# Optimization experiments

Hardware: AMD Instinct MI355X
Metric: run time of the kernel (lower is better)

The kernel has to match this reference:

```python
import jax, jax.numpy as jnp
import numpy as np
import math

N_HEAD = 16

def _rope(x):
    # x: [B, H, T, D], D even; interleaved-pair rotation as in the torch code
    B, H, T, D = x.shape
    theta = 10000.0 ** (-2.0 * jnp.arange(D // 2, dtype=x.dtype) / D)  # [D/2]
    pos = jnp.arange(T, dtype=x.dtype)[:, None]                        # [T,1]
    ang = pos * theta[None, :]                                          # [T, D/2]
    sin, cos = jnp.sin(ang), jnp.cos(ang)
    x1, x2 = x[..., ::2], x[..., 1::2]
    x1r = x1 * cos - x2 * sin
    x2r = x1 * sin + x2 * cos
    # re-interleave
    out = jnp.stack([x1r, x2r], axis=-1).reshape(B, H, T, D)
    return out

def setup_inputs() -> dict:
    key = jax.random.key(0)
    ks = jax.random.split(key, 3)
    B, T, C = 4, 2048, 1024
    x = jax.random.normal(ks[0], (B, T, C), dtype=jnp.float32)
    W_qkv = jax.random.normal(ks[1], (C, 3 * C), dtype=jnp.float32) * (1.0 / math.sqrt(C))
    b_qkv = jnp.zeros((3 * C,), dtype=jnp.float32)
    W_proj = jax.random.normal(ks[2], (C, C), dtype=jnp.float32) * (1.0 / math.sqrt(C))
    b_proj = jnp.zeros((C,), dtype=jnp.float32)
    return {"x": x, "W_qkv": W_qkv, "b_qkv": b_qkv, "W_proj": W_proj, "b_proj": b_proj}

def reference(x, W_qkv, b_qkv, W_proj, b_proj):
    B, T, C = x.shape
    H = N_HEAD
    D = C // H
    qkv = x @ W_qkv + b_qkv                      # [B,T,3C]
    q, k, v = jnp.split(qkv, 3, axis=-1)
    def to_heads(t):
        return t.reshape(B, T, H, D).transpose(0, 2, 1, 3)  # [B,H,T,D]
    q, k, v = to_heads(q), to_heads(k), to_heads(v)
    q = _rope(q)
    k = _rope(k)
    att = jnp.einsum('bhqd,bhkd->bhqk', q, k) * (1.0 / math.sqrt(D))
    mask = jnp.tril(jnp.ones((T, T), dtype=bool))
    att = jnp.where(mask[None, None, :, :], att, -jnp.inf)
    att = jax.nn.softmax(att, axis=-1)
    y = jnp.einsum('bhqk,bhkd->bhqd', att, v)    # [B,H,T,D]
    y = y.transpose(0, 2, 1, 3).reshape(B, T, C)
    return y @ W_proj + b_proj
```

## Files before the change

kernel.cpp:

```cpp
#include <hip/hip_runtime.h>
#include <cstddef>

#define B_DIM 4
#define T_DIM 2048
#define C_DIM 1024
#define H_DIM 16
#define D_DIM 64
#define C3_DIM 3072

typedef __attribute__((ext_vector_type(8))) _Float16 f16x8;
typedef __attribute__((ext_vector_type(4))) _Float16 f16x4;
typedef __attribute__((ext_vector_type(4))) float f32x4;

typedef const __attribute__((address_space(1))) unsigned int* gptr_t;
typedef __attribute__((address_space(3))) unsigned int* lptr_t;

#define QSCALE 0.180336850073f
#define NTHETA 0.41524101186f

__global__ __launch_bounds__(256) void prep(
    const float* __restrict__ x, _Float16* __restrict__ xh,
    const float* __restrict__ Wq, _Float16* __restrict__ Wqt,
    const float* __restrict__ Wp, _Float16* __restrict__ Wpt)
{
    __shared__ float tile[64][65];
    const int z = blockIdx.x, tid = threadIdx.x;

    if (z < 8192) {
        size_t i = (size_t)z * 1024 + tid * 4;
        float4 v = *(const float4*)&x[i];
        f16x4 o = { (_Float16)v.x, (_Float16)v.y, (_Float16)v.z, (_Float16)v.w };
        *(f16x4*)&xh[i] = o;
        return;
    }

    const float* W;
    _Float16* Wt;
    int N, idx;
    if (z < 8960) { W = Wq; Wt = Wqt; N = C3_DIM; idx = z - 8192; }
    else          { W = Wp; Wt = Wpt; N = C_DIM;  idx = z - 8960; }
    const int K = C_DIM;
    const int nblk = N / 64;
    const int n0 = (idx % nblk) * 64, k0 = (idx / nblk) * 64;

    const int tx = tid & 15, ty = tid >> 4;
#pragma unroll
    for (int it = 0; it < 4; ++it) {
        int r = it * 16 + ty;
        *(float4*)&tile[r][tx * 4] =
            *(const float4*)&W[(size_t)(k0 + r) * N + n0 + tx * 4];
    }
    __syncthreads();
    int c = tid >> 2, t0 = (tid & 3) * 16;
    __align__(16) _Float16 tmp[16];
#pragma unroll
    for (int j = 0; j < 16; ++j) tmp[j] = (_Float16)tile[t0 + j][c];
    _Float16* o = Wt + (size_t)(n0 + c) * K + k0 + t0;
    *(f16x8*)o = *(f16x8*)&tmp[0];
    *(f16x8*)(o + 8) = *(f16x8*)&tmp[8];
}

#define STAGE8(BUF, KK)                                                       \
    do {                                                                      \
        __builtin_amdgcn_global_load_lds((gptr_t)(const void*)(ag + (KK)),    \
            (lptr_t)(void*)&Af[BUF][0][w * 2 + 0][0][0], 16, 0, 0);           \
        __builtin_amdgcn_global_load_lds((gptr_t)(const void*)(ag + (KK) + 16 * K), \
            (lptr_t)(void*)&Af[BUF][0][w * 2 + 1][0][0], 16, 0, 0);           \
        __builtin_amdgcn_global_load_lds((gptr_t)(const void*)(ag + (KK) + 32), \
            (lptr_t)(void*)&Af[BUF][1][w * 2 + 0][0][0], 16, 0, 0);           \
        __builtin_amdgcn_global_load_lds((gptr_t)(const void*)(ag + (KK) + 32 + 16 * K), \
            (lptr_t)(void*)&Af[BUF][1][w * 2 + 1][0][0], 16, 0, 0);           \
        __builtin_amdgcn_global_load_lds((gptr_t)(const void*)(bg + (KK)),    \
            (lptr_t)(void*)&Bf[BUF][0][w * 2 + 0][0][0], 16, 0, 0);           \
        __builtin_amdgcn_global_load_lds((gptr_t)(const void*)(bg + (KK) + 16 * K), \
            (lptr_t)(void*)&Bf[BUF][0][w * 2 + 1][0][0], 16, 0, 0);           \
        __builtin_amdgcn_global_load_lds((gptr_t)(const void*)(bg + (KK) + 32), \
            (lptr_t)(void*)&Bf[BUF][1][w * 2 + 0][0][0], 16, 0, 0);           \
        __builtin_amdgcn_global_load_lds((gptr_t)(const void*)(bg + (KK) + 32 + 16 * K), \
            (lptr_t)(void*)&Bf[BUF][1][w * 2 + 1][0][0], 16, 0, 0);           \
    } while (0)

#define COMPUTE64(CUR, SWAPPED)                                               \
    do {                                                                      \
        _Pragma("unroll")                                                     \
        for (int s = 0; s < 2; ++s) {                                         \
            f16x8 av[4], bv[4];                                               \
            _Pragma("unroll")                                                 \
            for (int i = 0; i < 4; ++i) {                                     \
                av[i] = *(const f16x8*)&Af[CUR][s][wm * 4 + i][lane][0];      \
                bv[i] = *(const f16x8*)&Bf[CUR][s][wn * 4 + i][lane][0];      \
            }                                                                 \
            _Pragma("unroll")                                                 \
            for (int i = 0; i < 4; ++i)                                       \
                _Pragma("unroll")                                             \
                for (int j = 0; j < 4; ++j)                                   \
                    acc[i][j] = (SWAPPED)                                     \
                        ? __builtin_amdgcn_mfma_f32_16x16x32_f16(             \
                              bv[j], av[i], acc[i][j], 0, 0, 0)               \
                        : __builtin_amdgcn_mfma_f32_16x16x32_f16(             \
                              av[i], bv[j], acc[i][j], 0, 0, 0);              \
        }                                                                     \
    } while (0)

__global__ __launch_bounds__(256) void gemm_qkv(
    const _Float16* __restrict__ A, const _Float16* __restrict__ Bt,
    const float* __restrict__ bias,
    _Float16* __restrict__ Qb, _Float16* __restrict__ Kb, _Float16* __restrict__ Vt)
{
    __shared__ __align__(16) _Float16 Af[2][2][8][64][8];
    __shared__ __align__(16) _Float16 Bf[2][2][8][64][8];
    const int tid = threadIdx.x;
    const int lane = tid & 63, w = tid >> 6;
    const int lm = lane & 15, lq = lane >> 4;
    const int wm = w >> 1, wn = w & 1;
    const int m0 = blockIdx.y * 128, n0 = blockIdx.x * 128;
    const int K = C_DIM;

    const _Float16* ag = A + (size_t)(m0 + w * 32 + lm) * K + lq * 8;
    const _Float16* bg = Bt + (size_t)(n0 + w * 32 + lm) * K + lq * 8;

    f32x4 acc[4][4];
#pragma unroll
    for (int i = 0; i < 4; ++i)
#pragma unroll
        for (int j = 0; j < 4; ++j) acc[i][j] = (f32x4){0.f, 0.f, 0.f, 0.f};

    const bool is_v = (n0 >= 2 * C_DIM);

    if (!is_v) {
        STAGE8(0, 0);
        __syncthreads();
        int cur = 0;
        for (int kt = 0; kt < K / 64 - 1; ++kt) {
            STAGE8(cur ^ 1, (kt + 1) * 64);
            COMPUTE64(cur, true);
            __syncthreads();
            cur ^= 1;
        }
        COMPUTE64(cur, true);

        const bool is_q = (n0 < C_DIM);
        const float scale = is_q ? QSCALE : 1.0f;
        _Float16* dstbase = is_q ? Qb : Kb;
#pragma unroll
        for (int j = 0; j < 4; ++j) {
            int col = n0 + wn * 64 + j * 16 + lq * 4;
            int d0 = col & 63;
            int h = (col & (C_DIM - 1)) >> 6;
            float4 b4 = *(const float4*)&bias[col];
            float th0 = exp2f(-NTHETA * (float)(d0 >> 1));
            float th1 = exp2f(-NTHETA * (float)((d0 >> 1) + 1));
#pragma unroll
            for (int i = 0; i < 4; ++i) {
                int tg = m0 + wm * 64 + i * 16 + lm;
                int bb = tg >> 11, tl = tg & (T_DIM - 1);
                float v0 = acc[i][j][0] + b4.x;
                float v1 = acc[i][j][1] + b4.y;
                float v2 = acc[i][j][2] + b4.z;
                float v3 = acc[i][j][3] + b4.w;
                float s0, c0, s1, c1;
                __sincosf((float)tl * th0, &s0, &c0);
                __sincosf((float)tl * th1, &s1, &c1);
                f16x4 o = { (_Float16)((v0 * c0 - v1 * s0) * scale),
                            (_Float16)((v0 * s0 + v1 * c0) * scale),
                            (_Float16)((v2 * c1 - v3 * s1) * scale),
                            (_Float16)((v2 * s1 + v3 * c1) * scale) };
                *(f16x4*)&dstbase[((size_t)(bb * 16 + h) * T_DIM + tl) * 64 + d0] = o;
            }
        }
    } else {
        STAGE8(0, 0);
        __syncthreads();
        int cur = 0;
        for (int kt = 0; kt < K / 64 - 1; ++kt) {
            STAGE8(cur ^ 1, (kt + 1) * 64);
            COMPUTE64(cur, false);
            __syncthreads();
            cur ^= 1;
        }
        COMPUTE64(cur, false);

#pragma unroll
        for (int i = 0; i < 4; ++i) {
            int t4 = m0 + wm * 64 + i * 16 + lq * 4;
            int bb = t4 >> 11, tl = t4 & (T_DIM - 1);
#pragma unroll
            for (int j = 0; j < 4; ++j) {
                int col = n0 + wn * 64 + j * 16 + lm;
                int dfull = col - 2 * C_DIM;
                int h = dfull >> 6, d = dfull & 63;
                float bc = bias[col];
                f16x4 o = { (_Float16)(acc[i][j][0] + bc),
                            (_Float16)(acc[i][j][1] + bc),
                            (_Float16)(acc[i][j][2] + bc),
                            (_Float16)(acc[i][j][3] + bc) };
                *(f16x4*)&Vt[((size_t)(bb * 16 + h) * 64 + d) * T_DIM + tl] = o;
            }
        }
    }
}

template <bool OUT_HALF>
__global__ __launch_bounds__(256) void gemm_bt(
    const _Float16* __restrict__ A, const _Float16* __restrict__ Bt,
    const float* __restrict__ bias, void* __restrict__ Cout,
    int M, int N, int K)
{
    __shared__ __align__(16) _Float16 Af[2][2][8][64][8];
    __shared__ __align__(16) _Float16 Bf[2][2][8][64][8];
    const int tid = threadIdx.x;
    const int lane = tid & 63, w = tid >> 6;
    const int lm = lane & 15, lq = lane >> 4;
    const int wm = w >> 1, wn = w & 1;
    const int m0 = blockIdx.y * 128, n0 = blockIdx.x * 128;

    const _Float16* ag = A + (size_t)(m0 + w * 32 + lm) * K + lq * 8;
    const _Float16* bg = Bt + (size_t)(n0 + w * 32 + lm) * K + lq * 8;

    f32x4 acc[4][4];
#pragma unroll
    for (int i = 0; i < 4; ++i)
#pragma unroll
        for (int j = 0; j < 4; ++j) acc[i][j] = (f32x4){0.f, 0.f, 0.f, 0.f};

    STAGE8(0, 0);
    __syncthreads();
    int cur = 0;
    for (int kt = 0; kt < K / 64 - 1; ++kt) {
        STAGE8(cur ^ 1, (kt + 1) * 64);
        COMPUTE64(cur, true);
        __syncthreads();
        cur ^= 1;
    }
    COMPUTE64(cur, true);

#pragma unroll
    for (int i = 0; i < 4; ++i) {
        size_t row = (size_t)(m0 + wm * 64 + i * 16 + lm);
#pragma unroll
        for (int j = 0; j < 4; ++j) {
            int col = n0 + wn * 64 + j * 16 + lq * 4;
            float4 b4 = *(const float4*)&bias[col];
            float v0 = acc[i][j][0] + b4.x;
            float v1 = acc[i][j][1] + b4.y;
            float v2 = acc[i][j][2] + b4.z;
            float v3 = acc[i][j][3] + b4.w;
            if (OUT_HALF) {
                f16x4 o = { (_Float16)v0, (_Float16)v1, (_Float16)v2, (_Float16)v3 };
                *(f16x4*)&((_Float16*)Cout)[row * N + col] = o;
            } else {
                float4 o = make_float4(v0, v1, v2, v3);
                *(float4*)&((float*)Cout)[row * N + col] = o;
            }
        }
    }
}

__global__ __launch_bounds__(256) void attn_mfma(
    const _Float16* __restrict__ Qb, const _Float16* __restrict__ Kb,
    const _Float16* __restrict__ Vt, _Float16* __restrict__ yb)
{
    __shared__ __align__(16) _Float16 Kf[8][64][8];
    __shared__ __align__(16) _Float16 Vf[8][64][8];
    __shared__ __align__(16) _Float16 Pb[4][16][72];

    const int tid = threadIdx.x;
    const int bh = blockIdx.x;
    const int qt = 31 - blockIdx.y;
    const int b = bh >> 4, h = bh & 15;
    const int lane = tid & 63, w = tid >> 6;
    const int m = lane & 15, qq = lane >> 4;

    const _Float16* qrow = Qb +
        ((size_t)bh * T_DIM + qt * 64 + w * 16 + m) * D_DIM + qq * 8;
    f16x8 qreg[2];
    qreg[0] = *(const f16x8*)qrow;
    qreg[1] = *(const f16x8*)(qrow + 32);

    float m_i = -1e30f, l_i = 0.f;
    f32x4 acc[4];
#pragma unroll
    for (int db = 0; db < 4; ++db) acc[db] = (f32x4){0.f, 0.f, 0.f, 0.f};

    const _Float16* kg0 = Kb + (size_t)bh * T_DIM * D_DIM +
                          (size_t)(w * 16 + m) * D_DIM + qq * 8;
    const _Float16* vg0 = Vt + (size_t)bh * D_DIM * T_DIM +
                          (size_t)(w * 16 + m) * T_DIM + qq * 8;

    f16x8 kr0 = *(const f16x8*)(kg0);
    f16x8 kr1 = *(const f16x8*)(kg0 + 32);
    f16x8 vr0 = *(const f16x8*)(vg0);
    f16x8 vr1 = *(const f16x8*)(vg0 + 32);

    for (int kt = 0; kt <= qt; ++kt) {
        __syncthreads();
        *(f16x8*)&Kf[w * 2 + 0][lane][0] = kr0;
        *(f16x8*)&Kf[w * 2 + 1][lane][0] = kr1;
        *(f16x8*)&Vf[w * 2 + 0][lane][0] = vr0;
        *(f16x8*)&Vf[w * 2 + 1][lane][0] = vr1;
        __syncthreads();

        int ktn = (kt < qt) ? kt + 1 : kt;
        kr0 = *(const f16x8*)(kg0 + (size_t)ktn * 64 * D_DIM);
        kr1 = *(const f16x8*)(kg0 + (size_t)ktn * 64 * D_DIM + 32);
        vr0 = *(const f16x8*)(vg0 + ktn * 64);
        vr1 = *(const f16x8*)(vg0 + ktn * 64 + 32);

        f32x4 sv[4];
#pragma unroll
        for (int nb = 0; nb < 4; ++nb) {
            f32x4 s = (f32x4){0.f, 0.f, 0.f, 0.f};
            s = __builtin_amdgcn_mfma_f32_16x16x32_f16(
                *(const f16x8*)&Kf[nb * 2 + 0][lane][0], qreg[0], s, 0, 0, 0);
            s = __builtin_amdgcn_mfma_f32_16x16x32_f16(
                *(const f16x8*)&Kf[nb * 2 + 1][lane][0], qreg[1], s, 0, 0, 0);
            sv[nb] = s;
        }

        if (kt == qt) {
            int qlocal = w * 16 + m;
#pragma unroll
            for (int nb = 0; nb < 4; ++nb) {
                int tb = nb * 16 + qq * 4;
#pragma unroll
                for (int r = 0; r < 4; ++r)
                    if (tb + r > qlocal) sv[nb][r] = -1e30f;
            }
        }

        float mt0 = fmaxf(fmaxf(sv[0][0], sv[0][1]), fmaxf(sv[0][2], sv[0][3]));
        float mt1 = fmaxf(fmaxf(sv[1][0], sv[1][1]), fmaxf(sv[1][2], sv[1][3]));
        float mt2 = fmaxf(fmaxf(sv[2][0], sv[2][1]), fmaxf(sv[2][2], sv[2][3]));
        float mt3 = fmaxf(fmaxf(sv[3][0], sv[3][1]), fmaxf(sv[3][2], sv[3][3]));
        float mt = fmaxf(fmaxf(mt0, mt1), fmaxf(mt2, mt3));
        mt = fmaxf(mt, __shfl_xor(mt, 16));
        mt = fmaxf(mt, __shfl_xor(mt, 32));
        float mnew = fmaxf(m_i, mt);
        float alpha = exp2f(m_i - mnew);
        float ll = 0.f;
#pragma unroll
        for (int nb = 0; nb < 4; ++nb) {
            float p0 = exp2f(sv[nb][0] - mnew);
            float p1 = exp2f(sv[nb][1] - mnew);
            float p2 = exp2f(sv[nb][2] - mnew);
            float p3 = exp2f(sv[nb][3] - mnew);
            sv[nb][0] = p0; sv[nb][1] = p1; sv[nb][2] = p2; sv[nb][3] = p3;
            ll += (p0 + p1) + (p2 + p3);
        }
        ll += __shfl_xor(ll, 16);
        ll += __shfl_xor(ll, 32);
        l_i = l_i * alpha + ll;
        m_i = mnew;
#pragma unroll
        for (int db = 0; db < 4; ++db) {
            acc[db][0] *= alpha; acc[db][1] *= alpha;
            acc[db][2] *= alpha; acc[db][3] *= alpha;
        }

#pragma unroll
        for (int nb = 0; nb < 4; ++nb) {
            f16x4 pv = { (_Float16)sv[nb][0], (_Float16)sv[nb][1],
                         (_Float16)sv[nb][2], (_Float16)sv[nb][3] };
            *(f16x4*)&Pb[w][m][nb * 16 + qq * 4] = pv;
        }

        f16x8 pf0 = *(const f16x8*)&Pb[w][m][0 * 32 + qq * 8];
        f16x8 pf1 = *(const f16x8*)&Pb[w][m][1 * 32 + qq * 8];

#pragma unroll
        for (int db = 0; db < 4; ++db) {
            acc[db] = __builtin_amdgcn_mfma_f32_16x16x32_f16(
                *(const f16x8*)&Vf[db * 2 + 0][lane][0], pf0, acc[db], 0, 0, 0);
            acc[db] = __builtin_amdgcn_mfma_f32_16x16x32_f16(
                *(const f16x8*)&Vf[db * 2 + 1][lane][0], pf1, acc[db], 0, 0, 0);
        }
    }

    float inv = 1.0f / l_i;
    _Float16* yrow = yb + (size_t)(b * T_DIM + qt * 64 + w * 16 + m) * C_DIM +
                     h * D_DIM + qq * 4;
#pragma unroll
    for (int db = 0; db < 4; ++db) {
        f16x4 o = { (_Float16)(acc[db][0] * inv), (_Float16)(acc[db][1] * inv),
                    (_Float16)(acc[db][2] * inv), (_Float16)(acc[db][3] * inv) };
        *(f16x4*)(yrow + db * 16) = o;
    }
}

extern "C" void kernel_launch(void* const* d_in, const int* in_sizes, int n_in,
                              void* d_out, int out_size, void* d_ws, size_t ws_size,
                              hipStream_t stream)
{
    const float* x     = (const float*)d_in[0];
    const float* Wqkv  = (const float*)d_in[1];
    const float* bqkv  = (const float*)d_in[2];
    const float* Wproj = (const float*)d_in[3];
    const float* bproj = (const float*)d_in[4];
    float* out = (float*)d_out;

    char* ws = (char*)d_ws;
    _Float16* xh  = (_Float16*)(ws);
    _Float16* yh  = (_Float16*)(ws + 16777216ull);
    _Float16* Qb  = (_Float16*)(ws + 33554432ull);
    _Float16* Kb  = (_Float16*)(ws + 50331648ull);
    _Float16* Vt  = (_Float16*)(ws + 67108864ull);
    _Float16* Wqt = (_Float16*)(ws + 83886080ull);
    _Float16* Wpt = (_Float16*)(ws + 90177536ull);

    dim3 blk(256);

    prep<<<dim3(9216), blk, 0, stream>>>(x, xh, Wqkv, Wqt, Wproj, Wpt);

    gemm_qkv<<<dim3(C3_DIM / 128, (B_DIM * T_DIM) / 128), blk, 0, stream>>>(
        xh, Wqt, bqkv, Qb, Kb, Vt);

    attn_mfma<<<dim3(B_DIM * H_DIM, T_DIM / 64), blk, 0, stream>>>(
        Qb, Kb, Vt, yh);

    gemm_bt<false><<<dim3(C_DIM / 128, (B_DIM * T_DIM) / 128), blk, 0, stream>>>(
        yh, Wpt, bproj, out, B_DIM * T_DIM, C_DIM, C_DIM);
}
```

Measured before the change: 334.7 us.

## Halve GEMM k-tile to 32 and use partial vmcnt waits with raw barriers

Shrinks the per-stage K tile from 64 to 32, halving LDS usage per block, and rewrites the double-buffered main loop. It now issues the next stage's async global-to-LDS loads, waits only for the previous stage with a partial vmcnt, and syncs with raw s_barrier instead of __syncthreads. The aim is better overlap of loads with MFMA and possibly higher occupancy, at the cost of twice as many loop iterations and barriers per GEMM.

```diff
diff --git a/kernel.cpp b/kernel.cpp
--- a/kernel.cpp
+++ b/kernel.cpp
@@ -60,46 +60,54 @@
     *(f16x8*)(o + 8) = *(f16x8*)&tmp[8];
 }
 
-#define STAGE8(BUF, KK)                                                       \
+#define STAGE4(BUF, KK)                                                       \
     do {                                                                      \
         __builtin_amdgcn_global_load_lds((gptr_t)(const void*)(ag + (KK)),    \
-            (lptr_t)(void*)&Af[BUF][0][w * 2 + 0][0][0], 16, 0, 0);           \
-        __builtin_amdgcn_global_load_lds((gptr_t)(const void*)(ag + (KK) + 16 * K), \
-            (lptr_t)(void*)&Af[BUF][0][w * 2 + 1][0][0], 16, 0, 0);           \
-        __builtin_amdgcn_global_load_lds((gptr_t)(const void*)(ag + (KK) + 32), \
-            (lptr_t)(void*)&Af[BUF][1][w * 2 + 0][0][0], 16, 0, 0);           \
-        __builtin_amdgcn_global_load_lds((gptr_t)(const void*)(ag + (KK) + 32 + 16 * K), \
-            (lptr_t)(void*)&Af[BUF][1][w * 2 + 1][0][0], 16, 0, 0);           \
+            (lptr_t)(void*)&Af[BUF][w * 2 + 0][0][0], 16, 0, 0);              \
+        __builtin_amdgcn_global_load_lds(                                     \
+            (gptr_t)(const void*)(ag + (KK) + 16 * K),                        \
+            (lptr_t)(void*)&Af[BUF][w * 2 + 1][0][0], 16, 0, 0);              \
         __builtin_amdgcn_global_load_lds((gptr_t)(const void*)(bg + (KK)),    \
-            (lptr_t)(void*)&Bf[BUF][0][w * 2 + 0][0][0], 16, 0, 0);           \
-        __builtin_amdgcn_global_load_lds((gptr_t)(const void*)(bg + (KK) + 16 * K), \
-            (lptr_t)(void*)&Bf[BUF][0][w * 2 + 1][0][0], 16, 0, 0);           \
-        __builtin_amdgcn_global_load_lds((gptr_t)(const void*)(bg + (KK) + 32), \
-            (lptr_t)(void*)&Bf[BUF][1][w * 2 + 0][0][0], 16, 0, 0);           \
-        __builtin_amdgcn_global_load_lds((gptr_t)(const void*)(bg + (KK) + 32 + 16 * K), \
-            (lptr_t)(void*)&Bf[BUF][1][w * 2 + 1][0][0], 16, 0, 0);           \
+            (lptr_t)(void*)&Bf[BUF][w * 2 + 0][0][0], 16, 0, 0);              \
+        __builtin_amdgcn_global_load_lds(                                     \
+            (gptr_t)(const void*)(bg + (KK) + 16 * K),                        \
+            (lptr_t)(void*)&Bf[BUF][w * 2 + 1][0][0], 16, 0, 0);              \
     } while (0)
 
-#define COMPUTE64(CUR, SWAPPED)                                               \
+#define COMPUTE32(CUR, SWAPPED)                                               \
     do {                                                                      \
+        f16x8 av[4], bv[4];                                                   \
         _Pragma("unroll")                                                     \
-        for (int s = 0; s < 2; ++s) {                                         \
-            f16x8 av[4], bv[4];                                               \
+        for (int i = 0; i < 4; ++i) {                                         \
+            av[i] = *(const f16x8*)&Af[CUR][wm * 4 + i][lane][0];             \
+            bv[i] = *(const f16x8*)&Bf[CUR][wn * 4 + i][lane][0];             \
+        }                                                                     \
+        _Pragma("unroll")                                                     \
+        for (int i = 0; i < 4; ++i)                                           \
             _Pragma("unroll")                                                 \
-            for (int i = 0; i < 4; ++i) {                                     \
-                av[i] = *(const f16x8*)&Af[CUR][s][wm * 4 + i][lane][0];      \
-                bv[i] = *(const f16x8*)&Bf[CUR][s][wn * 4 + i][lane][0];      \
-            }                                                                 \
-            _Pragma("unroll")                                                 \
-            for (int i = 0; i < 4; ++i)                                       \
-                _Pragma("unroll")                                             \
-                for (int j = 0; j < 4; ++j)                                   \
-                    acc[i][j] = (SWAPPED)                                     \
-                        ? __builtin_amdgcn_mfma_f32_16x16x32_f16(             \
-                              bv[j], av[i], acc[i][j], 0, 0, 0)               \
-                        : __builtin_amdgcn_mfma_f32_16x16x32_f16(             \
-                              av[i], bv[j], acc[i][j], 0, 0, 0);              \
+            for (int j = 0; j < 4; ++j)                                       \
+                acc[i][j] = (SWAPPED)                                         \
+                    ? __builtin_amdgcn_mfma_f32_16x16x32_f16(                 \
+                          bv[j], av[i], acc[i][j], 0, 0, 0)                   \
+                    : __builtin_amdgcn_mfma_f32_16x16x32_f16(                 \
+                          av[i], bv[j], acc[i][j], 0, 0, 0);                  \
+    } while (0)
+
+#define KLOOP(SWAPPED)                                                        \
+    do {                                                                      \
+        STAGE4(0, 0);                                                         \
+        int cur = 0;                                                          \
+        for (int kt = 0; kt < K / 32 - 1; ++kt) {                             \
+            STAGE4(cur ^ 1, (kt + 1) * 32);                                   \
+            asm volatile("s_waitcnt vmcnt(4)" ::: "memory");                  \
+            __builtin_amdgcn_s_barrier();                                     \
+            COMPUTE32(cur, SWAPPED);                                          \
+            __builtin_amdgcn_s_barrier();                                     \
+            cur ^= 1;                                                         \
         }                                                                     \
+        asm volatile("s_waitcnt vmcnt(0)" ::: "memory");                      \
+        __builtin_amdgcn_s_barrier();                                         \
+        COMPUTE32(cur, SWAPPED);                                              \
     } while (0)
 
 __global__ __launch_bounds__(256) void gemm_qkv(
@@ -107,8 +115,8 @@
     const float* __restrict__ bias,
     _Float16* __restrict__ Qb, _Float16* __restrict__ Kb, _Float16* __restrict__ Vt)
 {
-    __shared__ __align__(16) _Float16 Af[2][2][8][64][8];
-    __shared__ __align__(16) _Float16 Bf[2][2][8][64][8];
+    __shared__ __align__(16) _Float16 Af[2][8][64][8];
+    __shared__ __align__(16) _Float16 Bf[2][8][64][8];
     const int tid = threadIdx.x;
     const int lane = tid & 63, w = tid >> 6;
     const int lm = lane & 15, lq = lane >> 4;
@@ -128,16 +136,7 @@
     const bool is_v = (n0 >= 2 * C_DIM);
 
     if (!is_v) {
-        STAGE8(0, 0);
-        __syncthreads();
-        int cur = 0;
-        for (int kt = 0; kt < K / 64 - 1; ++kt) {
-            STAGE8(cur ^ 1, (kt + 1) * 64);
-            COMPUTE64(cur, true);
-            __syncthreads();
-            cur ^= 1;
-        }
-        COMPUTE64(cur, true);
+        KLOOP(true);
 
         const bool is_q = (n0 < C_DIM);
         const float scale = is_q ? QSCALE : 1.0f;
@@ -169,16 +168,7 @@
             }
         }
     } else {
-        STAGE8(0, 0);
-        __syncthreads();
-        int cur = 0;
-        for (int kt = 0; kt < K / 64 - 1; ++kt) {
-            STAGE8(cur ^ 1, (kt + 1) * 64);
-            COMPUTE64(cur, false);
-            __syncthreads();
-            cur ^= 1;
-        }
-        COMPUTE64(cur, false);
+        KLOOP(false);
 
 #pragma unroll
         for (int i = 0; i < 4; ++i) {
@@ -206,8 +196,8 @@
     const float* __restrict__ bias, void* __restrict__ Cout,
     int M, int N, int K)
 {
-    __shared__ __align__(16) _Float16 Af[2][2][8][64][8];
-    __shared__ __align__(16) _Float16 Bf[2][2][8][64][8];
+    __shared__ __align__(16) _Float16 Af[2][8][64][8];
+    __shared__ __align__(16) _Float16 Bf[2][8][64][8];
     const int tid = threadIdx.x;
     const int lane = tid & 63, w = tid >> 6;
     const int lm = lane & 15, lq = lane >> 4;
@@ -223,16 +213,7 @@
 #pragma unroll
         for (int j = 0; j < 4; ++j) acc[i][j] = (f32x4){0.f, 0.f, 0.f, 0.f};
 
-    STAGE8(0, 0);
-    __syncthreads();
-    int cur = 0;
-    for (int kt = 0; kt < K / 64 - 1; ++kt) {
-        STAGE8(cur ^ 1, (kt + 1) * 64);
-        COMPUTE64(cur, true);
-        __syncthreads();
-        cur ^= 1;
-    }
-    COMPUTE64(cur, true);
+    KLOOP(true);
 
 #pragma unroll
     for (int i = 0; i < 4; ++i) {
```

Result: faster. 313.8 us (-6.2%).
